# Kernel optimization log

Hardware: AMD Instinct MI355X
Metric: run time of the kernel (lower is better)

Reference implementation:

```python
import jax, jax.numpy as jnp
import numpy as np

B, S, E = 2, 2048, 1024
H = 16
D = E // H          # head dim = 64
K_TOP = 64          # top-k tokens kept per query in sparse branch
M = 256             # performer kernel feature dim
EPS = 1e-6


def setup_inputs() -> dict:
    key = jax.random.key(0)
    ks = jax.random.split(key, 16)
    sc = 0.02
    p = {
        'x': jax.random.normal(ks[0], (B, S, E), jnp.float32),
        # sparse-attention branch params
        'Wq_s': jax.random.normal(ks[1], (E, E), jnp.float32) * sc,
        'Wk_s': jax.random.normal(ks[2], (E, E), jnp.float32) * sc,
        'Wv_s': jax.random.normal(ks[3], (E, E), jnp.float32) * sc,
        'Wo_s': jax.random.normal(ks[4], (E, E), jnp.float32) * sc,
        'bq_s': jnp.zeros((E,), jnp.float32),
        'bk_s': jnp.zeros((E,), jnp.float32),
        'bv_s': jnp.zeros((E,), jnp.float32),
        'bo_s': jnp.zeros((E,), jnp.float32),
        # performer branch params
        'Wq_p': jax.random.normal(ks[5], (E, E), jnp.float32) * sc,
        'Wk_p': jax.random.normal(ks[6], (E, E), jnp.float32) * sc,
        'Wv_p': jax.random.normal(ks[7], (E, E), jnp.float32) * sc,
        'Wo_p': jax.random.normal(ks[8], (E, E), jnp.float32) * sc,
        'bo_p': jnp.zeros((E,), jnp.float32),
        'Wfeat': jax.random.normal(ks[9], (D, M), jnp.float32) / np.sqrt(D),
        # gate
        'Wg': jax.random.normal(ks[10], (E, 2), jnp.float32) * sc,
        'bg': jnp.zeros((2,), jnp.float32),
    }
    return p


def _split_heads(t):
    # [B,S,E] -> [B,H,S,D]
    return t.reshape(B, S, H, D).transpose(0, 2, 1, 3)


def _merge_heads(t):
    # [B,H,S,D] -> [B,S,E]
    return t.transpose(0, 2, 1, 3).reshape(B, S, E)


def _sparse_attn(x, Wq, bq, Wk, bk, Wv, bv, Wo, bo):
    q = _split_heads(x @ Wq + bq)
    k = _split_heads(x @ Wk + bk)
    v = _split_heads(x @ Wv + bv)
    scores = jnp.einsum('bhqd,bhkd->bhqk', q, k) / np.sqrt(D)  # [B,H,S,S]
    # keep only top-K scores per query row
    topv = jax.lax.top_k(scores, K_TOP)[0]
    thresh = topv[..., -1:]
    neg = jnp.finfo(scores.dtype).min
    masked = jnp.where(scores >= thresh, scores, neg)
    attn = jax.nn.softmax(masked, axis=-1)
    out = jnp.einsum('bhqk,bhkd->bhqd', attn, v)
    return _merge_heads(out) @ Wo + bo


def _performer_attn(x, Wq, Wk, Wv, Wo, bo, Wfeat):
    q = _split_heads(x @ Wq)
    k = _split_heads(x @ Wk)
    v = _split_heads(x @ Wv)
    # learned relu feature map (FAVOR-style linear attention)
    phi_q = jax.nn.relu(jnp.einsum('bhsd,dm->bhsm', q, Wfeat)) + EPS
    phi_k = jax.nn.relu(jnp.einsum('bhsd,dm->bhsm', k, Wfeat)) + EPS
    kv = jnp.einsum('bhsm,bhsd->bhmd', phi_k, v)      # [B,H,M,D]
    z = phi_k.sum(axis=2)                              # [B,H,M]
    num = jnp.einsum('bhsm,bhmd->bhsd', phi_q, kv)
    den = jnp.einsum('bhsm,bhm->bhs', phi_q, z)[..., None] + EPS
    return _merge_heads(num / den) @ Wo + bo


def reference(x, Wq_s, Wk_s, Wv_s, Wo_s, bq_s, bk_s, bv_s, bo_s,
              Wq_p, Wk_p, Wv_p, Wo_p, bo_p, Wfeat, Wg, bg):
    sparse_out = _sparse_attn(x, Wq_s, bq_s, Wk_s, bk_s, Wv_s, bv_s, Wo_s, bo_s)
    perf_out = _performer_attn(x, Wq_p, Wk_p, Wv_p, Wo_p, bo_p, Wfeat)
    avg_hidden = x.mean(axis=1)                        # [B,E]
    gate = jax.nn.softmax(avg_hidden @ Wg + bg, axis=-1)  # [B,2]
    w_s = gate[:, 0][:, None, None]
    w_p = gate[:, 1][:, None, None]
    # dropout is identity in eval/reference mode
    return w_s * sparse_out + w_p * perf_out
```

## Files before the change

### kernel.cpp

```cpp
#include <hip/hip_runtime.h>


constexpr int cB = 2, cS = 2048, cE = 1024, cH = 16, cD = 64, cKTOP = 64, cM = 256;
constexpr float cEPS = 1e-6f;

typedef _Float16 half8 __attribute__((ext_vector_type(8)));
typedef float f32x16 __attribute__((ext_vector_type(16)));

__device__ __forceinline__ unsigned int f2key(float f) {
    unsigned int u = __float_as_uint(f);
    return (u & 0x80000000u) ? ~u : (u | 0x80000000u);
}

__device__ __forceinline__ unsigned short h2u(_Float16 h) {
    union { _Float16 h; unsigned short u; } x; x.h = h; return x.u;
}

__device__ __forceinline__ half8 ld_half8(const unsigned short* p) {
    union { uint4 u; half8 h; } x;
    x.u = *(const uint4*)p;
    return x.h;
}

__global__ __launch_bounds__(256)
void gemm_qk2_blas(const float* __restrict__ A,
                   const float* __restrict__ Wq,
                   const float* __restrict__ Wk,
                   const float* __restrict__ bq,
                   const float* __restrict__ bk_,
                   float* __restrict__ Cq,
                   float* __restrict__ Ck,
                   unsigned short* __restrict__ khi,
                   int K, int N)
{
    __shared__ __align__(16) float As[16][68];
    __shared__ __align__(16) float Bq[16][68];
    __shared__ __align__(16) float Bk[16][68];
    const int t  = threadIdx.x;
    const int r0 = blockIdx.y * 64;
    const int c0 = blockIdx.x * 64;
    const int tm = t >> 4, tn = t & 15;
    float paccQ[4][4] = {};
    float caccQ[4][4] = {};
    float paccK[4][4] = {};
    float caccK[4][4] = {};

    const int ar = t >> 2, ak = (t & 3) * 4;
    const int bk = t >> 4, bc = (t & 15) * 4;

    for (int k0 = 0; k0 < K; k0 += 16) {
        const float4 av  = *(const float4*)(A  + (size_t)(r0 + ar) * K + (k0 + ak));
        const float4 bqv = *(const float4*)(Wq + (size_t)(k0 + bk) * N + (c0 + bc));
        const float4 bkv = *(const float4*)(Wk + (size_t)(k0 + bk) * N + (c0 + bc));
        As[ak + 0][ar] = av.x;
        As[ak + 1][ar] = av.y;
        As[ak + 2][ar] = av.z;
        As[ak + 3][ar] = av.w;
        *(float4*)&Bq[bk][bc] = bqv;
        *(float4*)&Bk[bk][bc] = bkv;
        __syncthreads();
        #pragma unroll
        for (int kk = 0; kk < 16; ++kk) {
            const float4 a4  = *(const float4*)&As[kk][tm * 4];
            const float4 q4  = *(const float4*)&Bq[kk][tn * 4];
            const float4 k4  = *(const float4*)&Bk[kk][tn * 4];
            const float a[4]  = {a4.x, a4.y, a4.z, a4.w};
            const float bqr[4] = {q4.x, q4.y, q4.z, q4.w};
            const float bkr[4] = {k4.x, k4.y, k4.z, k4.w};
            #pragma unroll
            for (int i = 0; i < 4; ++i)
                #pragma unroll
                for (int j = 0; j < 4; ++j) {
                    paccQ[i][j] = fmaf(a[i], bqr[j], paccQ[i][j]);
                    paccK[i][j] = fmaf(a[i], bkr[j], paccK[i][j]);
                }
        }
        __syncthreads();
        const int kn = k0 + 16;
        if (kn == 384 || kn == 768 || kn == K) {
            #pragma unroll
            for (int i = 0; i < 4; ++i)
                #pragma unroll
                for (int j = 0; j < 4; ++j) {
                    caccQ[i][j] = caccQ[i][j] + paccQ[i][j];
                    paccQ[i][j] = 0.f;
                    caccK[i][j] = caccK[i][j] + paccK[i][j];
                    paccK[i][j] = 0.f;
                }
        }
    }
    #pragma unroll
    for (int i = 0; i < 4; ++i) {
        const int r = r0 + tm * 4 + i;
        const int c = c0 + tn * 4;
        float4 vq;
        vq.x = caccQ[i][0] + bq[c + 0];
        vq.y = caccQ[i][1] + bq[c + 1];
        vq.z = caccQ[i][2] + bq[c + 2];
        vq.w = caccQ[i][3] + bq[c + 3];
        *(float4*)&Cq[(size_t)r * N + c] = vq;
        float4 vk;
        vk.x = caccK[i][0] + bk_[c + 0];
        vk.y = caccK[i][1] + bk_[c + 1];
        vk.z = caccK[i][2] + bk_[c + 2];
        vk.w = caccK[i][3] + bk_[c + 3];
        *(float4*)&Ck[(size_t)r * N + c] = vk;
        ushort4 hs;
        hs.x = h2u((_Float16)vk.x);
        hs.y = h2u((_Float16)vk.y);
        hs.z = h2u((_Float16)vk.z);
        hs.w = h2u((_Float16)vk.w);
        *(ushort4*)&khi[(size_t)r * N + c] = hs;
    }
}

__global__ __launch_bounds__(256)
void conv_wT(const float* __restrict__ W,
             unsigned short* __restrict__ wthi,
             unsigned short* __restrict__ wtlo)
{
    __shared__ float tile[64][68];
    const int t  = threadIdx.x;
    const int k0 = blockIdx.y * 64;
    const int n0 = blockIdx.x * 64;
    const int r  = t >> 4, c4 = (t & 15) * 4;
    #pragma unroll
    for (int i = 0; i < 4; ++i) {
        const int k = r + 16 * i;
        const float4 v = *(const float4*)&W[(size_t)(k0 + k) * cE + n0 + c4];
        tile[k][c4 + 0] = v.x; tile[k][c4 + 1] = v.y;
        tile[k][c4 + 2] = v.z; tile[k][c4 + 3] = v.w;
    }
    __syncthreads();
    #pragma unroll
    for (int i = 0; i < 4; ++i) {
        const int n = r + 16 * i;
        unsigned int hp[2], lp[2];
        #pragma unroll
        for (int p = 0; p < 2; ++p) {
            unsigned short hh[2], ll[2];
            #pragma unroll
            for (int j = 0; j < 2; ++j) {
                const float f = tile[c4 + p * 2 + j][n];
                const _Float16 h = (_Float16)f;
                hh[j] = h2u(h);
                ll[j] = h2u((_Float16)(f - (float)h));
            }
            hp[p] = (unsigned int)hh[0] | ((unsigned int)hh[1] << 16);
            lp[p] = (unsigned int)ll[0] | ((unsigned int)ll[1] << 16);
        }
        uint2 hv, lv;
        hv.x = hp[0]; hv.y = hp[1];
        lv.x = lp[0]; lv.y = lp[1];
        *(uint2*)&wthi[(size_t)(n0 + n) * cE + k0 + c4] = hv;
        *(uint2*)&wtlo[(size_t)(n0 + n) * cE + k0 + c4] = lv;
    }
}

__global__ __launch_bounds__(256)
void gemm_hilo(const float* __restrict__ A,
               const unsigned short* __restrict__ wthi,
               const unsigned short* __restrict__ wtlo,
               const float* __restrict__ bias,
               float* __restrict__ C)
{
    __shared__ __align__(16) unsigned short Ah[128][24];
    __shared__ __align__(16) unsigned short Al[128][24];
    __shared__ __align__(16) unsigned short Bh[64][24];
    __shared__ __align__(16) unsigned short Bl[64][24];

    const int t    = threadIdx.x;
    const int lane = t & 63, wave = t >> 6;
    const int wr   = wave >> 1, wc = wave & 1;
    const int r0   = blockIdx.y * 128, c0 = blockIdx.x * 64;
    const int fr   = lane & 31, g5 = lane >> 5;

    const int arow = t >> 1, aka = (t & 1) * 8;
    const int bsel = t >> 7;
    const int brow = (t & 127) >> 1, bkb = (t & 1) * 8;
    const unsigned short* wsrc = bsel ? wtlo : wthi;

    f32x16 acc0 = {0.f,0.f,0.f,0.f,0.f,0.f,0.f,0.f,0.f,0.f,0.f,0.f,0.f,0.f,0.f,0.f};
    f32x16 acc1 = {0.f,0.f,0.f,0.f,0.f,0.f,0.f,0.f,0.f,0.f,0.f,0.f,0.f,0.f,0.f,0.f};

    for (int k0 = 0; k0 < cE; k0 += 16) {
        const float4 x0 = *(const float4*)&A[(size_t)(r0 + arow) * cE + k0 + aka];
        const float4 x1 = *(const float4*)&A[(size_t)(r0 + arow) * cE + k0 + aka + 4];
        const float xf[8] = {x0.x, x0.y, x0.z, x0.w, x1.x, x1.y, x1.z, x1.w};
        unsigned int hw[4], lw[4];
        #pragma unroll
        for (int p = 0; p < 4; ++p) {
            unsigned short hh[2], ll[2];
            #pragma unroll
            for (int j = 0; j < 2; ++j) {
                const float f = xf[p * 2 + j];
                const _Float16 h = (_Float16)f;
                hh[j] = h2u(h);
                ll[j] = h2u((_Float16)(f - (float)h));
            }
            hw[p] = (unsigned int)hh[0] | ((unsigned int)hh[1] << 16);
            lw[p] = (unsigned int)ll[0] | ((unsigned int)ll[1] << 16);
        }
        uint4 hv, lv;
        hv.x = hw[0]; hv.y = hw[1]; hv.z = hw[2]; hv.w = hw[3];
        lv.x = lw[0]; lv.y = lw[1]; lv.z = lw[2]; lv.w = lw[3];
        *(uint4*)&Ah[arow][aka] = hv;
        *(uint4*)&Al[arow][aka] = lv;

        const uint4 wv = *(const uint4*)&wsrc[(size_t)(c0 + brow) * cE + k0 + bkb];
        if (bsel) *(uint4*)&Bl[brow][bkb] = wv;
        else      *(uint4*)&Bh[brow][bkb] = wv;
        __syncthreads();

        const half8 a0h = ld_half8(&Ah[wr * 64 + fr][g5 * 8]);
        const half8 a0l = ld_half8(&Al[wr * 64 + fr][g5 * 8]);
        const half8 a1h = ld_half8(&Ah[wr * 64 + 32 + fr][g5 * 8]);
        const half8 a1l = ld_half8(&Al[wr * 64 + 32 + fr][g5 * 8]);
        const half8 bh  = ld_half8(&Bh[wc * 32 + fr][g5 * 8]);
        const half8 bl  = ld_half8(&Bl[wc * 32 + fr][g5 * 8]);

        acc0 = __builtin_amdgcn_mfma_f32_32x32x16_f16(a0l, bh, acc0, 0, 0, 0);
        acc0 = __builtin_amdgcn_mfma_f32_32x32x16_f16(a0h, bl, acc0, 0, 0, 0);
        acc0 = __builtin_amdgcn_mfma_f32_32x32x16_f16(a0h, bh, acc0, 0, 0, 0);
        acc1 = __builtin_amdgcn_mfma_f32_32x32x16_f16(a1l, bh, acc1, 0, 0, 0);
        acc1 = __builtin_amdgcn_mfma_f32_32x32x16_f16(a1h, bl, acc1, 0, 0, 0);
        acc1 = __builtin_amdgcn_mfma_f32_32x32x16_f16(a1h, bh, acc1, 0, 0, 0);
        __syncthreads();
    }

    const int col = c0 + wc * 32 + fr;
    const float bv = bias ? bias[col] : 0.f;
    #pragma unroll
    for (int rg = 0; rg < 16; ++rg) {
        const int row = r0 + wr * 64 + (rg & 3) + 8 * (rg >> 2) + 4 * g5;
        C[(size_t)row * cE + col] = acc0[rg] + bv;
    }
    #pragma unroll
    for (int rg = 0; rg < 16; ++rg) {
        const int row = r0 + wr * 64 + 32 + (rg & 3) + 8 * (rg >> 2) + 4 * g5;
        C[(size_t)row * cE + col] = acc1[rg] + bv;
    }
}

__global__ __launch_bounds__(256)
void out_gemm_hilo(const float* __restrict__ As_, const float* __restrict__ Ap_,
                   const unsigned short* __restrict__ w1hi,
                   const unsigned short* __restrict__ w1lo,
                   const unsigned short* __restrict__ w2hi,
                   const unsigned short* __restrict__ w2lo,
                   const float* __restrict__ bos, const float* __restrict__ bop,
                   const float* __restrict__ gates, float* __restrict__ out)
{
    __shared__ __align__(16) unsigned short A1h[128][24], A1l[128][24];
    __shared__ __align__(16) unsigned short A2h[128][24], A2l[128][24];
    __shared__ __align__(16) unsigned short B1h[64][24],  B1l[64][24];
    __shared__ __align__(16) unsigned short B2h[64][24],  B2l[64][24];

    const int t    = threadIdx.x;
    const int lane = t & 63, wave = t >> 6;
    const int wr   = wave >> 1, wc = wave & 1;
    const int r0   = blockIdx.y * 128, c0 = blockIdx.x * 64;
    const int fr   = lane & 31, g5 = lane >> 5;
    const int b    = r0 >> 11;
    const float gs = gates[b * 2 + 0], gp = gates[b * 2 + 1];

    const int arow = t >> 1, aka = (t & 1) * 8;
    const int bsel = t >> 7;
    const int brow = (t & 127) >> 1, bkb = (t & 1) * 8;
    const unsigned short* s1 = bsel ? w1lo : w1hi;
    const unsigned short* s2 = bsel ? w2lo : w2hi;

    f32x16 acc0 = {0.f,0.f,0.f,0.f,0.f,0.f,0.f,0.f,0.f,0.f,0.f,0.f,0.f,0.f,0.f,0.f};
    f32x16 acc1 = {0.f,0.f,0.f,0.f,0.f,0.f,0.f,0.f,0.f,0.f,0.f,0.f,0.f,0.f,0.f,0.f};

    for (int k0 = 0; k0 < cE; k0 += 16) {
        {
            const float4 x0 = *(const float4*)&As_[(size_t)(r0 + arow) * cE + k0 + aka];
            const float4 x1 = *(const float4*)&As_[(size_t)(r0 + arow) * cE + k0 + aka + 4];
            const float xf[8] = {x0.x * gs, x0.y * gs, x0.z * gs, x0.w * gs,
                                 x1.x * gs, x1.y * gs, x1.z * gs, x1.w * gs};
            unsigned int hw[4], lw[4];
            #pragma unroll
            for (int p = 0; p < 4; ++p) {
                unsigned short hh[2], ll[2];
                #pragma unroll
                for (int j = 0; j < 2; ++j) {
                    const float f = xf[p * 2 + j];
                    const _Float16 h = (_Float16)f;
                    hh[j] = h2u(h);
                    ll[j] = h2u((_Float16)(f - (float)h));
                }
                hw[p] = (unsigned int)hh[0] | ((unsigned int)hh[1] << 16);
                lw[p] = (unsigned int)ll[0] | ((unsigned int)ll[1] << 16);
            }
            uint4 hv, lv;
            hv.x = hw[0]; hv.y = hw[1]; hv.z = hw[2]; hv.w = hw[3];
            lv.x = lw[0]; lv.y = lw[1]; lv.z = lw[2]; lv.w = lw[3];
            *(uint4*)&A1h[arow][aka] = hv;
            *(uint4*)&A1l[arow][aka] = lv;
        }
        {
            const float4 x0 = *(const float4*)&Ap_[(size_t)(r0 + arow) * cE + k0 + aka];
            const float4 x1 = *(const float4*)&Ap_[(size_t)(r0 + arow) * cE + k0 + aka + 4];
            const float xf[8] = {x0.x * gp, x0.y * gp, x0.z * gp, x0.w * gp,
                                 x1.x * gp, x1.y * gp, x1.z * gp, x1.w * gp};
            unsigned int hw[4], lw[4];
            #pragma unroll
            for (int p = 0; p < 4; ++p) {
                unsigned short hh[2], ll[2];
                #pragma unroll
                for (int j = 0; j < 2; ++j) {
                    const float f = xf[p * 2 + j];
                    const _Float16 h = (_Float16)f;
                    hh[j] = h2u(h);
                    ll[j] = h2u((_Float16)(f - (float)h));
                }
                hw[p] = (unsigned int)hh[0] | ((unsigned int)hh[1] << 16);
                lw[p] = (unsigned int)ll[0] | ((unsigned int)ll[1] << 16);
            }
            uint4 hv, lv;
            hv.x = hw[0]; hv.y = hw[1]; hv.z = hw[2]; hv.w = hw[3];
            lv.x = lw[0]; lv.y = lw[1]; lv.z = lw[2]; lv.w = lw[3];
            *(uint4*)&A2h[arow][aka] = hv;
            *(uint4*)&A2l[arow][aka] = lv;
        }
        {
            const uint4 w1 = *(const uint4*)&s1[(size_t)(c0 + brow) * cE + k0 + bkb];
            if (bsel) *(uint4*)&B1l[brow][bkb] = w1;
            else      *(uint4*)&B1h[brow][bkb] = w1;
            const uint4 w2 = *(const uint4*)&s2[(size_t)(c0 + brow) * cE + k0 + bkb];
            if (bsel) *(uint4*)&B2l[brow][bkb] = w2;
            else      *(uint4*)&B2h[brow][bkb] = w2;
        }
        __syncthreads();

        const half8 b1h = ld_half8(&B1h[wc * 32 + fr][g5 * 8]);
        const half8 b1l = ld_half8(&B1l[wc * 32 + fr][g5 * 8]);
        const half8 b2h = ld_half8(&B2h[wc * 32 + fr][g5 * 8]);
        const half8 b2l = ld_half8(&B2l[wc * 32 + fr][g5 * 8]);
        {
            const half8 a1h = ld_half8(&A1h[wr * 64 + fr][g5 * 8]);
            const half8 a1l = ld_half8(&A1l[wr * 64 + fr][g5 * 8]);
            const half8 a2h = ld_half8(&A2h[wr * 64 + fr][g5 * 8]);
            const half8 a2l = ld_half8(&A2l[wr * 64 + fr][g5 * 8]);
            acc0 = __builtin_amdgcn_mfma_f32_32x32x16_f16(a1l, b1h, acc0, 0, 0, 0);
            acc0 = __builtin_amdgcn_mfma_f32_32x32x16_f16(a1h, b1l, acc0, 0, 0, 0);
            acc0 = __builtin_amdgcn_mfma_f32_32x32x16_f16(a1h, b1h, acc0, 0, 0, 0);
            acc0 = __builtin_amdgcn_mfma_f32_32x32x16_f16(a2l, b2h, acc0, 0, 0, 0);
            acc0 = __builtin_amdgcn_mfma_f32_32x32x16_f16(a2h, b2l, acc0, 0, 0, 0);
            acc0 = __builtin_amdgcn_mfma_f32_32x32x16_f16(a2h, b2h, acc0, 0, 0, 0);
        }
        {
            const half8 a1h = ld_half8(&A1h[wr * 64 + 32 + fr][g5 * 8]);
            const half8 a1l = ld_half8(&A1l[wr * 64 + 32 + fr][g5 * 8]);
            const half8 a2h = ld_half8(&A2h[wr * 64 + 32 + fr][g5 * 8]);
            const half8 a2l = ld_half8(&A2l[wr * 64 + 32 + fr][g5 * 8]);
            acc1 = __builtin_amdgcn_mfma_f32_32x32x16_f16(a1l, b1h, acc1, 0, 0, 0);
            acc1 = __builtin_amdgcn_mfma_f32_32x32x16_f16(a1h, b1l, acc1, 0, 0, 0);
            acc1 = __builtin_amdgcn_mfma_f32_32x32x16_f16(a1h, b1h, acc1, 0, 0, 0);
            acc1 = __builtin_amdgcn_mfma_f32_32x32x16_f16(a2l, b2h, acc1, 0, 0, 0);
            acc1 = __builtin_amdgcn_mfma_f32_32x32x16_f16(a2h, b2l, acc1, 0, 0, 0);
            acc1 = __builtin_amdgcn_mfma_f32_32x32x16_f16(a2h, b2h, acc1, 0, 0, 0);
        }
        __syncthreads();
    }

    const int col = c0 + wc * 32 + fr;
    const float bv = gs * bos[col] + gp * bop[col];
    #pragma unroll
    for (int rg = 0; rg < 16; ++rg) {
        const int row = r0 + wr * 64 + (rg & 3) + 8 * (rg >> 2) + 4 * g5;
        out[(size_t)row * cE + col] = acc0[rg] + bv;
    }
    #pragma unroll
    for (int rg = 0; rg < 16; ++rg) {
        const int row = r0 + wr * 64 + 32 + (rg & 3) + 8 * (rg >> 2) + 4 * g5;
        out[(size_t)row * cE + col] = acc1[rg] + bv;
    }
}

__global__ __launch_bounds__(256, 4)
void sparse_attn(const float* __restrict__ Q,
                 const unsigned short* __restrict__ Khi,
                 const float* __restrict__ Ks, const float* __restrict__ V,
                 float* __restrict__ O)
{
    __shared__ float QfT[64][8];
    __shared__ __align__(16) unsigned short Qhi[8][72];
    __shared__ unsigned int hist[8][257];
    __shared__ unsigned short cidx[8][128];
    __shared__ double cval[8][128];
    __shared__ float cw[8][128];
    __shared__ int cnt[8];
    __shared__ int t16hi[8], rem[8], t16[8];
    __shared__ double T64s[8], s65s[8], rowm[8];

    const int t   = threadIdx.x;
    const int bh  = blockIdx.y;
    const int b   = bh >> 4;
    const int h64 = (bh & 15) * 64;
    const int q0  = blockIdx.x * 8;

    if (t < 128) {
        const int r = t >> 4, c4 = (t & 15) * 4;
        const float4 v =
            *(const float4*)&Q[((size_t)(b * cS + q0 + r)) * cE + h64 + c4];
        const float f[4] = {v.x, v.y, v.z, v.w};
        #pragma unroll
        for (int i = 0; i < 4; ++i) {
            QfT[c4 + i][r] = f[i];
            Qhi[r][c4 + i] = h2u((_Float16)f[i]);
        }
    }
    for (int i = t; i < 8 * 257; i += 256) (&hist[0][0])[i] = 0u;
    if (t < 8) cnt[t] = 0;
    __syncthreads();

    const int lane = t & 63;
    const int wv   = t >> 6;
    const int col  = lane & 31;
    const int g5   = lane >> 5;
    const int r0   = g5 * 4;

    half8 ahi[4];
    {
        const int arow = col & 7;
        #pragma unroll
        for (int ks = 0; ks < 4; ++ks)
            ahi[ks] = ld_half8(&Qhi[arow][g5 * 8 + ks * 16]);
    }
    unsigned int su[16][2];
    {
        const size_t kbase = ((size_t)(b * cS + wv * 512 + col)) * cE + h64;
        #pragma unroll
        for (int tl = 0; tl < 16; ++tl) {
            const unsigned short* kh = Khi + kbase + (size_t)tl * 32 * cE;
            f32x16 acc = {0.f,0.f,0.f,0.f,0.f,0.f,0.f,0.f,
                          0.f,0.f,0.f,0.f,0.f,0.f,0.f,0.f};
            #pragma unroll
            for (int ks = 0; ks < 4; ++ks) {
                const half8 bh8 = ld_half8(kh + g5 * 8 + ks * 16);
                acc = __builtin_amdgcn_mfma_f32_32x32x16_f16(ahi[ks], bh8, acc, 0, 0, 0);
            }
            const unsigned int k0 = f2key(acc[0] * 0.125f) >> 16;
            const unsigned int k1 = f2key(acc[1] * 0.125f) >> 16;
            const unsigned int k2 = f2key(acc[2] * 0.125f) >> 16;
            const unsigned int k3 = f2key(acc[3] * 0.125f) >> 16;
            su[tl][0] = k0 | (k1 << 16);
            su[tl][1] = k2 | (k3 << 16);
            atomicAdd(&hist[r0 + 0][k0 >> 8], 1u);
            atomicAdd(&hist[r0 + 1][k1 >> 8], 1u);
            atomicAdd(&hist[r0 + 2][k2 >> 8], 1u);
            atomicAdd(&hist[r0 + 3][k3 >> 8], 1u);
        }
    }
    __syncthreads();
    if (t < 8) {
        int need = cKTOP + 1;
        int hb = 0;
        for (int bin = 255; bin >= 0; --bin) {
            const int c = (int)hist[t][bin];
            if (c >= need) { hb = bin; break; }
            need -= c;
        }
        t16hi[t] = hb;
        rem[t] = need;
    }
    __syncthreads();
    for (int i = t; i < 8 * 257; i += 256) (&hist[0][0])[i] = 0u;
    __syncthreads();
    #pragma unroll
    for (int tl = 0; tl < 16; ++tl)
        #pragma unroll
        for (int w = 0; w < 2; ++w) {
            const unsigned int u = su[tl][w];
            const int rlo = r0 + 2 * w, rhi = rlo + 1;
            const unsigned int vlo = u & 0xFFFFu;
            const unsigned int vhi = u >> 16;
            if ((int)(vlo >> 8) == t16hi[rlo]) atomicAdd(&hist[rlo][vlo & 255u], 1u);
            if ((int)(vhi >> 8) == t16hi[rhi]) atomicAdd(&hist[rhi][vhi & 255u], 1u);
        }
    __syncthreads();
    if (t < 8) {
        int need = rem[t];
        int lb = 0;
        for (int bin = 255; bin >= 0; --bin) {
            const int c = (int)hist[t][bin];
            if (c >= need) { lb = bin; break; }
            need -= c;
        }
        t16[t] = (t16hi[t] << 8) | lb;
    }
    __syncthreads();

    #pragma unroll
    for (int tl = 0; tl < 16; ++tl) {
        const int key = wv * 512 + tl * 32 + col;
        #pragma unroll
        for (int w = 0; w < 2; ++w) {
            const unsigned int u = su[tl][w];
            const int rlo = r0 + 2 * w, rhi = rlo + 1;
            const int v0 = (int)(u & 0xFFFFu);
            const int v1 = (int)(u >> 16);
            if (v0 >= max(t16[rlo] - 3, 0)) {
                const int slot = atomicAdd(&cnt[rlo], 1);
                if (slot < 128) cidx[rlo][slot] = (unsigned short)key;
            }
            if (v1 >= max(t16[rhi] - 3, 0)) {
                const int slot = atomicAdd(&cnt[rhi], 1);
                if (slot < 128) cidx[rhi][slot] = (unsigned short)key;
            }
        }
    }
    __syncthreads();

    #pragma unroll
    for (int rx = 0; rx < 2; ++rx) {
        const int rr = wv * 2 + rx;
        const int n = min(cnt[rr], 128);
        for (int c = lane; c < n; c += 64) {
            const int key = cidx[rr][c];
            const float* kp = Ks + ((size_t)(b * cS + key)) * cE + h64;
            double a = 0.0;
            #pragma unroll 4
            for (int d4 = 0; d4 < 64; d4 += 4) {
                const float4 kv = *(const float4*)&kp[d4];
                a = fma((double)QfT[d4 + 0][rr], (double)kv.x, a);
                a = fma((double)QfT[d4 + 1][rr], (double)kv.y, a);
                a = fma((double)QfT[d4 + 2][rr], (double)kv.z, a);
                a = fma((double)QfT[d4 + 3][rr], (double)kv.w, a);
            }
            cval[rr][c] = a * 0.125;
        }
    }
    __syncthreads();

    #pragma unroll
    for (int rx = 0; rx < 2; ++rx) {
        const int rr = wv * 2 + rx;
        const int n = min(cnt[rr], 128);
        for (int c = lane; c < n; c += 64) {
            const double v = cval[rr][c];
            int rank = 0;
            for (int i = 0; i < n; ++i) rank += (cval[rr][i] > v) ? 1 : 0;
            if (rank == 0)  rowm[rr] = v;
            if (rank == 63) T64s[rr] = v;
            if (rank == 64) s65s[rr] = v;
        }
    }
    __syncthreads();

    #pragma unroll
    for (int rx = 0; rx < 2; ++rx) {
        const int rr = wv * 2 + rx;
        const int n = min(cnt[rr], 128);
        const double T64 = T64s[rr], s65 = s65s[rr], m = rowm[rr];
        float za = 0.f;
        for (int c = lane; c < n; c += 64) {
            const double v = cval[rr][c];
            if (v >= T64) za += expf((float)(v - m));
        }
        #pragma unroll
        for (int off = 32; off >= 1; off >>= 1)
            za += __shfl_xor(za, off);
        const float g   = (float)(T64 - s65);
        const float gm  = fmaxf(g - 5e-7f, 0.f);
        const float wB  = 0.5f * erfcf(gm * (1.0f / 2.2e-6f));
        const float wA  = 1.f - wB;
        const float e64 = expf((float)(T64 - m));
        const float e65 = expf((float)(s65 - m));
        const float ZB  = za - e64 + e65;
        const float cIn = wA / za + wB / ZB;
        const float c64 = wA / za;
        const float c65 = wB / ZB;
        for (int c = lane; c < n; c += 64) {
            const double v = cval[rr][c];
            float cc = 0.f;
            if (v > T64)       cc = cIn;
            else if (v == T64) cc = c64;
            else if (v == s65) cc = c65;
            cw[rr][c] = (cc != 0.f) ? cc * expf((float)(v - m)) : 0.f;
        }
    }
    __syncthreads();

    #pragma unroll
    for (int rx = 0; rx < 2; ++rx) {
        const int rr = wv * 2 + rx;
        const int n = min(cnt[rr], 128);
        float o = 0.f;
        int j = 0;
        for (; j + 8 <= n; j += 8) {
            float wreg[8];
            int   kreg[8];
            #pragma unroll
            for (int u = 0; u < 8; ++u) {
                wreg[u] = cw[rr][j + u];
                kreg[u] = cidx[rr][j + u];
            }
            float vreg[8];
            #pragma unroll
            for (int u = 0; u < 8; ++u)
                vreg[u] = V[((size_t)(b * cS + kreg[u])) * cE + h64 + lane];
            #pragma unroll
            for (int u = 0; u < 8; ++u)
                o = fmaf(wreg[u], vreg[u], o);
        }
        for (; j < n; ++j)
            o = fmaf(cw[rr][j],
                     V[((size_t)(b * cS + cidx[rr][j])) * cE + h64 + lane], o);
        O[((size_t)(b * cS + q0 + rr)) * cE + h64 + lane] = o;
    }
}

__global__ __launch_bounds__(256)
void perf_kv(const float* __restrict__ Kp, const float* __restrict__ Vp,
             const float* __restrict__ Wfeat,
             float* __restrict__ kvpart, float* __restrict__ zpart)
{
    __shared__ __align__(16) float Wf[64][68];
    __shared__ __align__(16) float Kt[64][68];
    __shared__ __align__(16) float Vt[64][68];
    __shared__ __align__(16) float Ph[64][68];
    const int t    = threadIdx.x;
    const int mc   = blockIdx.x & 3;
    const int sc   = blockIdx.x >> 2;
    const int bh   = blockIdx.y;
    const int b    = bh >> 4;
    const int h64  = (bh & 15) * 64;
    const int m0   = mc * 64;
    const int sbase = sc * 1024;

    #pragma unroll
    for (int i = 0; i < 4; ++i) {
        const int lin = t + 256 * i;
        const int d   = lin >> 4;
        const int m4  = (lin & 15) * 4;
        *(float4*)&Wf[d][m4] = *(const float4*)&Wfeat[d * cM + m0 + m4];
    }

    const int tm = t >> 4, tn = t & 15;
    const int sr = tm * 4;
    const int cn = tn * 4;
    float akv[4][4] = {};
    float az = 0.f;

    for (int st = 0; st < 16; ++st) {
        const int s0g = sbase + st * 64;
        __syncthreads();
        #pragma unroll
        for (int i = 0; i < 4; ++i) {
            const int row = tm + 16 * i;
            const size_t base = ((size_t)(b * cS + s0g + row)) * cE + h64 + cn;
            *(float4*)&Kt[row][cn] = *(const float4*)&Kp[base];
            *(float4*)&Vt[row][cn] = *(const float4*)&Vp[base];
        }
        __syncthreads();
        float4 p0 = {0,0,0,0}, p1 = {0,0,0,0}, p2 = {0,0,0,0}, p3 = {0,0,0,0};
        #pragma unroll 8
        for (int d = 0; d < 64; ++d) {
            const float4 wv = *(const float4*)&Wf[d][cn];
            const float k0 = Kt[sr + 0][d], k1 = Kt[sr + 1][d];
            const float k2 = Kt[sr + 2][d], k3 = Kt[sr + 3][d];
            p0.x = fmaf(k0, wv.x, p0.x); p0.y = fmaf(k0, wv.y, p0.y);
            p0.z = fmaf(k0, wv.z, p0.z); p0.w = fmaf(k0, wv.w, p0.w);
            p1.x = fmaf(k1, wv.x, p1.x); p1.y = fmaf(k1, wv.y, p1.y);
            p1.z = fmaf(k1, wv.z, p1.z); p1.w = fmaf(k1, wv.w, p1.w);
            p2.x = fmaf(k2, wv.x, p2.x); p2.y = fmaf(k2, wv.y, p2.y);
            p2.z = fmaf(k2, wv.z, p2.z); p2.w = fmaf(k2, wv.w, p2.w);
            p3.x = fmaf(k3, wv.x, p3.x); p3.y = fmaf(k3, wv.y, p3.y);
            p3.z = fmaf(k3, wv.z, p3.z); p3.w = fmaf(k3, wv.w, p3.w);
        }
        p0.x = fmaxf(p0.x, 0.f) + cEPS; p0.y = fmaxf(p0.y, 0.f) + cEPS;
        p0.z = fmaxf(p0.z, 0.f) + cEPS; p0.w = fmaxf(p0.w, 0.f) + cEPS;
        p1.x = fmaxf(p1.x, 0.f) + cEPS; p1.y = fmaxf(p1.y, 0.f) + cEPS;
        p1.z = fmaxf(p1.z, 0.f) + cEPS; p1.w = fmaxf(p1.w, 0.f) + cEPS;
        p2.x = fmaxf(p2.x, 0.f) + cEPS; p2.y = fmaxf(p2.y, 0.f) + cEPS;
        p2.z = fmaxf(p2.z, 0.f) + cEPS; p2.w = fmaxf(p2.w, 0.f) + cEPS;
        p3.x = fmaxf(p3.x, 0.f) + cEPS; p3.y = fmaxf(p3.y, 0.f) + cEPS;
        p3.z = fmaxf(p3.z, 0.f) + cEPS; p3.w = fmaxf(p3.w, 0.f) + cEPS;
        *(float4*)&Ph[sr + 0][cn] = p0;
        *(float4*)&Ph[sr + 1][cn] = p1;
        *(float4*)&Ph[sr + 2][cn] = p2;
        *(float4*)&Ph[sr + 3][cn] = p3;
        __syncthreads();
        #pragma unroll 8
        for (int ss = 0; ss < 64; ++ss) {
            const float4 pv = *(const float4*)&Ph[ss][sr];
            const float4 vv = *(const float4*)&Vt[ss][cn];
            akv[0][0] = fmaf(pv.x, vv.x, akv[0][0]); akv[0][1] = fmaf(pv.x, vv.y, akv[0][1]);
            akv[0][2] = fmaf(pv.x, vv.z, akv[0][2]); akv[0][3] = fmaf(pv.x, vv.w, akv[0][3]);
            akv[1][0] = fmaf(pv.y, vv.x, akv[1][0]); akv[1][1] = fmaf(pv.y, vv.y, akv[1][1]);
            akv[1][2] = fmaf(pv.y, vv.z, akv[1][2]); akv[1][3] = fmaf(pv.y, vv.w, akv[1][3]);
            akv[2][0] = fmaf(pv.z, vv.x, akv[2][0]); akv[2][1] = fmaf(pv.z, vv.y, akv[2][1]);
            akv[2][2] = fmaf(pv.z, vv.z, akv[2][2]); akv[2][3] = fmaf(pv.z, vv.w, akv[2][3]);
            akv[3][0] = fmaf(pv.w, vv.x, akv[3][0]); akv[3][1] = fmaf(pv.w, vv.y, akv[3][1]);
            akv[3][2] = fmaf(pv.w, vv.z, akv[3][2]); akv[3][3] = fmaf(pv.w, vv.w, akv[3][3]);
        }
        if (t < 64) {
            float a = 0.f;
            #pragma unroll 8
            for (int ss = 0; ss < 64; ++ss) a += Ph[ss][t];
            az += a;
        }
    }
    const size_t obase = ((size_t)(sc * 32 + bh)) * cM + m0;
    #pragma unroll
    for (int i = 0; i < 4; ++i) {
        float4 v; v.x = akv[i][0]; v.y = akv[i][1]; v.z = akv[i][2]; v.w = akv[i][3];
        *(float4*)&kvpart[(obase + sr + i) * cD + cn] = v;
    }
    if (t < 64) zpart[obase + t] = az;
}

__global__ __launch_bounds__(256)
void perf_numden(const float* __restrict__ Qp, const float* __restrict__ Wfeat,
                 const float* __restrict__ kvpart, const float* __restrict__ zpart,
                 float* __restrict__ Ap)
{
    __shared__ __align__(16) float Wf[64][68];
    __shared__ __align__(16) float Qt[64][68];
    __shared__ __align__(16) float KV[64][68];
    __shared__ __align__(16) float Ph[64][68];
    __shared__ __align__(16) float zl[64];
    __shared__ float den[64];
    const int t   = threadIdx.x;
    const int stb = blockIdx.x;
    const int bh  = blockIdx.y;
    const int b   = bh >> 4;
    const int h64 = (bh & 15) * 64;
    const int s0  = stb * 64;
    const int tm  = t >> 4, tn = t & 15;
    const int sr  = tm * 4, cn = tn * 4;

    #pragma unroll
    for (int i = 0; i < 4; ++i) {
        const int row = tm + 16 * i;
        *(float4*)&Qt[row][cn] =
            *(const float4*)&Qp[((size_t)(b * cS + s0 + row)) * cE + h64 + cn];
    }

    float num[4][4] = {};
    float dacc = 0.f;

    for (int mc = 0; mc < 4; ++mc) {
        const int m0 = mc * 64;
        __syncthreads();
        #pragma unroll
        for (int i = 0; i < 4; ++i) {
            const int lin = t + 256 * i;
            const int d   = lin >> 4;
            const int m4  = (lin & 15) * 4;
            *(float4*)&Wf[d][m4] = *(const float4*)&Wfeat[d * cM + m0 + m4];
        }
        #pragma unroll
        for (int i = 0; i < 4; ++i) {
            const int row = tm + 16 * i;
            const size_t o0 = ((size_t)bh * cM + m0 + row) * cD + cn;
            const size_t o1 = ((size_t)(32 + bh) * cM + m0 + row) * cD + cn;
            const float4 a = *(const float4*)&kvpart[o0];
            const float4 c = *(const float4*)&kvpart[o1];
            float4 v; v.x = a.x + c.x; v.y = a.y + c.y; v.z = a.z + c.z; v.w = a.w + c.w;
            *(float4*)&KV[row][cn] = v;
        }
        if (t < 64)
            zl[t] = zpart[(size_t)bh * cM + m0 + t] + zpart[(size_t)(32 + bh) * cM + m0 + t];
        __syncthreads();
        float4 p0 = {0,0,0,0}, p1 = {0,0,0,0}, p2 = {0,0,0,0}, p3 = {0,0,0,0};
        #pragma unroll 8
        for (int d = 0; d < 64; ++d) {
            const float4 wv = *(const float4*)&Wf[d][cn];
            const float q0 = Qt[sr + 0][d], q1 = Qt[sr + 1][d];
            const float q2 = Qt[sr + 2][d], q3 = Qt[sr + 3][d];
            p0.x = fmaf(q0, wv.x, p0.x); p0.y = fmaf(q0, wv.y, p0.y);
            p0.z = fmaf(q0, wv.z, p0.z); p0.w = fmaf(q0, wv.w, p0.w);
            p1.x = fmaf(q1, wv.x, p1.x); p1.y = fmaf(q1, wv.y, p1.y);
            p1.z = fmaf(q1, wv.z, p1.z); p1.w = fmaf(q1, wv.w, p1.w);
            p2.x = fmaf(q2, wv.x, p2.x); p2.y = fmaf(q2, wv.y, p2.y);
            p2.z = fmaf(q2, wv.z, p2.z); p2.w = fmaf(q2, wv.w, p2.w);
            p3.x = fmaf(q3, wv.x, p3.x); p3.y = fmaf(q3, wv.y, p3.y);
            p3.z = fmaf(q3, wv.z, p3.z); p3.w = fmaf(q3, wv.w, p3.w);
        }
        p0.x = fmaxf(p0.x, 0.f) + cEPS; p0.y = fmaxf(p0.y, 0.f) + cEPS;
        p0.z = fmaxf(p0.z, 0.f) + cEPS; p0.w = fmaxf(p0.w, 0.f) + cEPS;
        p1.x = fmaxf(p1.x, 0.f) + cEPS; p1.y = fmaxf(p1.y, 0.f) + cEPS;
        p1.z = fmaxf(p1.z, 0.f) + cEPS; p1.w = fmaxf(p1.w, 0.f) + cEPS;
        p2.x = fmaxf(p2.x, 0.f) + cEPS; p2.y = fmaxf(p2.y, 0.f) + cEPS;
        p2.z = fmaxf(p2.z, 0.f) + cEPS; p2.w = fmaxf(p2.w, 0.f) + cEPS;
        p3.x = fmaxf(p3.x, 0.f) + cEPS; p3.y = fmaxf(p3.y, 0.f) + cEPS;
        p3.z = fmaxf(p3.z, 0.f) + cEPS; p3.w = fmaxf(p3.w, 0.f) + cEPS;
        *(float4*)&Ph[sr + 0][cn] = p0;
        *(float4*)&Ph[sr + 1][cn] = p1;
        *(float4*)&Ph[sr + 2][cn] = p2;
        *(float4*)&Ph[sr + 3][cn] = p3;
        __syncthreads();
        #pragma unroll 8
        for (int mm = 0; mm < 64; ++mm) {
            const float4 kvv = *(const float4*)&KV[mm][cn];
            const float a0 = Ph[sr + 0][mm], a1 = Ph[sr + 1][mm];
            const float a2 = Ph[sr + 2][mm], a3 = Ph[sr + 3][mm];
            num[0][0] = fmaf(a0, kvv.x, num[0][0]); num[0][1] = fmaf(a0, kvv.y, num[0][1]);
            num[0][2] = fmaf(a0, kvv.z, num[0][2]); num[0][3] = fmaf(a0, kvv.w, num[0][3]);
            num[1][0] = fmaf(a1, kvv.x, num[1][0]); num[1][1] = fmaf(a1, kvv.y, num[1][1]);
            num[1][2] = fmaf(a1, kvv.z, num[1][2]); num[1][3] = fmaf(a1, kvv.w, num[1][3]);
            num[2][0] = fmaf(a2, kvv.x, num[2][0]); num[2][1] = fmaf(a2, kvv.y, num[2][1]);
            num[2][2] = fmaf(a2, kvv.z, num[2][2]); num[2][3] = fmaf(a2, kvv.w, num[2][3]);
            num[3][0] = fmaf(a3, kvv.x, num[3][0]); num[3][1] = fmaf(a3, kvv.y, num[3][1]);
            num[3][2] = fmaf(a3, kvv.z, num[3][2]); num[3][3] = fmaf(a3, kvv.w, num[3][3]);
        }
        if (t < 64) {
            float a = 0.f;
            #pragma unroll
            for (int m4 = 0; m4 < 64; m4 += 4) {
                const float4 ph = *(const float4*)&Ph[t][m4];
                const float4 zz = *(const float4*)&zl[m4];
                a = fmaf(ph.x, zz.x, a); a = fmaf(ph.y, zz.y, a);
                a = fmaf(ph.z, zz.z, a); a = fmaf(ph.w, zz.w, a);
            }
            dacc += a;
        }
    }
    __syncthreads();
    if (t < 64) den[t] = dacc + cEPS;
    __syncthreads();
    #pragma unroll
    for (int i = 0; i < 4; ++i) {
        const float di = 1.f / den[sr + i];
        float4 v;
        v.x = num[i][0] * di; v.y = num[i][1] * di;
        v.z = num[i][2] * di; v.w = num[i][3] * di;
        *(float4*)&Ap[((size_t)(b * cS + s0 + sr + i)) * cE + h64 + cn] = v;
    }
}

__global__ __launch_bounds__(256)
void gate_avg(const float* __restrict__ x, double* __restrict__ avgpart)
{
    const int i  = blockIdx.x * 256 + threadIdx.x;
    const int sc = blockIdx.y;
    const int b  = i >> 10, e = i & 1023;
    double acc = 0.0;
    const int sEnd = sc * 128 + 128;
    for (int s = sc * 128; s < sEnd; ++s)
        acc += (double)x[((size_t)(b * cS + s)) * cE + e];
    avgpart[(size_t)sc * 2048 + i] = acc;
}

__global__ void gate_final(const double* __restrict__ avgpart, const float* __restrict__ Wg,
                           const float* __restrict__ bg, float* __restrict__ gates)
{
    const int t = threadIdx.x;
    const int b = t >> 6, lane = t & 63;
    float l0 = 0.f, l1 = 0.f;
    for (int e = lane; e < cE; e += 64) {
        double s = 0.0;
        #pragma unroll
        for (int sc = 0; sc < 16; ++sc)
            s += avgpart[(size_t)sc * 2048 + b * 1024 + e];
        const float a = (float)(s / (double)cS);
        l0 = fmaf(a, Wg[e * 2 + 0], l0);
        l1 = fmaf(a, Wg[e * 2 + 1], l1);
    }
    for (int off = 32; off >= 1; off >>= 1) {
        l0 += __shfl_down(l0, off);
        l1 += __shfl_down(l1, off);
    }
    if (lane == 0) {
        l0 += bg[0]; l1 += bg[1];
        const float m = fmaxf(l0, l1);
        const float e0 = expf(l0 - m), e1 = expf(l1 - m);
        const float s = e0 + e1;
        gates[b * 2 + 0] = e0 / s;
        gates[b * 2 + 1] = e1 / s;
    }
}

extern "C" void kernel_launch(void* const* d_in, const int* in_sizes, int n_in,
                              void* d_out, int out_size, void* d_ws, size_t ws_size,
                              hipStream_t stream)
{
    (void)in_sizes; (void)n_in; (void)out_size; (void)ws_size;
    const float* x     = (const float*)d_in[0];
    const float* Wq_s  = (const float*)d_in[1];
    const float* Wk_s  = (const float*)d_in[2];
    const float* Wv_s  = (const float*)d_in[3];
    const float* Wo_s  = (const float*)d_in[4];
    const float* bq_s  = (const float*)d_in[5];
    const float* bk_s  = (const float*)d_in[6];
    const float* bv_s  = (const float*)d_in[7];
    const float* bo_s  = (const float*)d_in[8];
    const float* Wq_p  = (const float*)d_in[9];
    const float* Wk_p  = (const float*)d_in[10];
    const float* Wv_p  = (const float*)d_in[11];
    const float* Wo_p  = (const float*)d_in[12];
    const float* bo_p  = (const float*)d_in[13];
    const float* Wfeat = (const float*)d_in[14];
    const float* Wg    = (const float*)d_in[15];
    const float* bg    = (const float*)d_in[16];

    float* ws = (float*)d_ws;
    const size_t NRE = (size_t)cB * cS * cE;
    float* Qs    = ws;
    float* Ks    = Qs + NRE;
    float* KsT   = Ks + NRE;
    float* Vs    = KsT + NRE;
    float* Asout = Vs + NRE;
    float* kvpart = Asout + NRE;
    float* zpart  = kvpart + (size_t)2 * 32 * cM * cD;
    double* avgpart = (double*)(zpart + (size_t)2 * 32 * cM);
    float* gates = (float*)(avgpart + (size_t)16 * 2048);
    unsigned short* wthi  = (unsigned short*)(gates + 16);
    unsigned short* wtlo  = wthi + (size_t)cE * cE;
    unsigned short* wo1hi = wtlo + (size_t)cE * cE;
    unsigned short* wo1lo = wo1hi + (size_t)cE * cE;
    unsigned short* wo2hi = wo1lo + (size_t)cE * cE;
    unsigned short* wo2lo = wo2hi + (size_t)cE * cE;

    unsigned short* Khi = (unsigned short*)KsT;

    conv_wT<<<dim3(16, 16), 256, 0, stream>>>(Wo_s, wo1hi, wo1lo);
    conv_wT<<<dim3(16, 16), 256, 0, stream>>>(Wo_p, wo2hi, wo2lo);

    gemm_qk2_blas<<<dim3(16, 64), 256, 0, stream>>>(x, Wq_s, Wk_s, bq_s, bk_s,
                                                    Qs, Ks, Khi, cE, cE);
    conv_wT<<<dim3(16, 16), 256, 0, stream>>>(Wv_s, wthi, wtlo);
    gemm_hilo<<<dim3(16, 32), 256, 0, stream>>>(x, wthi, wtlo, bv_s, Vs);
    sparse_attn<<<dim3(256, 32), 256, 0, stream>>>(Qs, Khi, Ks, Vs, Asout);

    float* Qp    = Qs;
    float* Kp    = Ks;
    float* Vp    = Vs;
    float* Apout = KsT;
    conv_wT<<<dim3(16, 16), 256, 0, stream>>>(Wq_p, wthi, wtlo);
    gemm_hilo<<<dim3(16, 32), 256, 0, stream>>>(x, wthi, wtlo, nullptr, Qp);
    conv_wT<<<dim3(16, 16), 256, 0, stream>>>(Wk_p, wthi, wtlo);
    gemm_hilo<<<dim3(16, 32), 256, 0, stream>>>(x, wthi, wtlo, nullptr, Kp);
    conv_wT<<<dim3(16, 16), 256, 0, stream>>>(Wv_p, wthi, wtlo);
    gemm_hilo<<<dim3(16, 32), 256, 0, stream>>>(x, wthi, wtlo, nullptr, Vp);
    perf_kv<<<dim3(8, 32), 256, 0, stream>>>(Kp, Vp, Wfeat, kvpart, zpart);
    perf_numden<<<dim3(32, 32), 256, 0, stream>>>(Qp, Wfeat, kvpart, zpart, Apout);

    gate_avg<<<dim3(8, 16), 256, 0, stream>>>(x, avgpart);
    gate_final<<<dim3(1), 128, 0, stream>>>(avgpart, Wg, bg, gates);
    out_gemm_hilo<<<dim3(16, 32), 256, 0, stream>>>(Asout, Apout,
                                                    wo1hi, wo1lo, wo2hi, wo2lo,
                                                    bo_s, bo_p, gates,
                                                    (float*)d_out);
}
```

Baseline: 1.398 ms.

## Split sparse attention into candidate-selection and exact-attention kernels

The fused sparse attention kernel is split in two. The first kernel runs the fp16 MFMA scoring and histogram threshold search, then writes up to 128 candidate key indices and a count per query row to global memory. The second kernel reloads those candidates and does the fp64 rescoring, top-k softmax and V accumulation with a lighter shared-memory footprint, so it can use a higher occupancy bound. In exchange it adds a kernel launch and a global round trip for the candidate lists, and it grows the workspace.

```diff
diff --git a/kernel.cpp b/kernel.cpp
--- a/kernel.cpp
+++ b/kernel.cpp
@@ -380,26 +380,22 @@
 }
 
 __global__ __launch_bounds__(256, 4)
-void sparse_attn(const float* __restrict__ Q,
-                 const unsigned short* __restrict__ Khi,
-                 const float* __restrict__ Ks, const float* __restrict__ V,
-                 float* __restrict__ O)
-{
-    __shared__ float QfT[64][8];
+void sparse_sel(const float* __restrict__ Q,
+                const unsigned short* __restrict__ Khi,
+                unsigned short* __restrict__ gcidx,
+                int* __restrict__ gcnt)
+{
     __shared__ __align__(16) unsigned short Qhi[8][72];
     __shared__ unsigned int hist[8][257];
-    __shared__ unsigned short cidx[8][128];
-    __shared__ double cval[8][128];
-    __shared__ float cw[8][128];
     __shared__ int cnt[8];
     __shared__ int t16hi[8], rem[8], t16[8];
-    __shared__ double T64s[8], s65s[8], rowm[8];
 
     const int t   = threadIdx.x;
     const int bh  = blockIdx.y;
     const int b   = bh >> 4;
     const int h64 = (bh & 15) * 64;
     const int q0  = blockIdx.x * 8;
+    const size_t rid0 = ((size_t)bh * 256 + blockIdx.x) * 8;
 
     if (t < 128) {
         const int r = t >> 4, c4 = (t & 15) * 4;
@@ -407,10 +403,8 @@
             *(const float4*)&Q[((size_t)(b * cS + q0 + r)) * cE + h64 + c4];
         const float f[4] = {v.x, v.y, v.z, v.w};
         #pragma unroll
-        for (int i = 0; i < 4; ++i) {
-            QfT[c4 + i][r] = f[i];
+        for (int i = 0; i < 4; ++i)
             Qhi[r][c4 + i] = h2u((_Float16)f[i]);
-        }
     }
     for (int i = t; i < 8 * 257; i += 256) (&hist[0][0])[i] = 0u;
     if (t < 8) cnt[t] = 0;
@@ -504,15 +498,51 @@
             const int v1 = (int)(u >> 16);
             if (v0 >= max(t16[rlo] - 3, 0)) {
                 const int slot = atomicAdd(&cnt[rlo], 1);
-                if (slot < 128) cidx[rlo][slot] = (unsigned short)key;
+                if (slot < 128) gcidx[(rid0 + rlo) * 128 + slot] = (unsigned short)key;
             }
             if (v1 >= max(t16[rhi] - 3, 0)) {
                 const int slot = atomicAdd(&cnt[rhi], 1);
-                if (slot < 128) cidx[rhi][slot] = (unsigned short)key;
+                if (slot < 128) gcidx[(rid0 + rhi) * 128 + slot] = (unsigned short)key;
             }
         }
     }
     __syncthreads();
+    if (t < 8) gcnt[rid0 + t] = cnt[t];
+}
+
+__global__ __launch_bounds__(256, 8)
+void sparse_att(const float* __restrict__ Q,
+                const unsigned short* __restrict__ gcidx,
+                const int* __restrict__ gcnt,
+                const float* __restrict__ Ks, const float* __restrict__ V,
+                float* __restrict__ O)
+{
+    __shared__ float QfT[64][8];
+    __shared__ unsigned short cidx[8][128];
+    __shared__ double cval[8][128];
+    __shared__ float cw[8][128];
+    __shared__ int cnt[8];
+    __shared__ double T64s[8], s65s[8], rowm[8];
+
+    const int t   = threadIdx.x;
+    const int bh  = blockIdx.y;
+    const int b   = bh >> 4;
+    const int h64 = (bh & 15) * 64;
+    const int q0  = blockIdx.x * 8;
+    const size_t rid0 = ((size_t)bh * 256 + blockIdx.x) * 8;
+
+    if (t < 128) {
+        const int r = t >> 4, c4 = (t & 15) * 4;
+        const float4 v =
+            *(const float4*)&Q[((size_t)(b * cS + q0 + r)) * cE + h64 + c4];
+        QfT[c4 + 0][r] = v.x; QfT[c4 + 1][r] = v.y;
+        QfT[c4 + 2][r] = v.z; QfT[c4 + 3][r] = v.w;
+    }
+    ((ushort4*)&cidx[0][0])[t] = ((const ushort4*)&gcidx[rid0 * 128])[t];
+    if (t < 8) cnt[t] = gcnt[rid0 + t];
+    __syncthreads();
+
+    const int wv = t >> 6, lane = t & 63;
 
     #pragma unroll
     for (int rx = 0; rx < 2; ++rx) {
@@ -915,6 +945,8 @@
     unsigned short* wo1lo = wo1hi + (size_t)cE * cE;
     unsigned short* wo2hi = wo1lo + (size_t)cE * cE;
     unsigned short* wo2lo = wo2hi + (size_t)cE * cE;
+    unsigned short* gcidx = wo2lo + (size_t)cE * cE;
+    int* gcnt = (int*)(gcidx + (size_t)256 * 32 * 8 * 128);
 
     unsigned short* Khi = (unsigned short*)KsT;
 
@@ -925,7 +957,8 @@
                                                     Qs, Ks, Khi, cE, cE);
     conv_wT<<<dim3(16, 16), 256, 0, stream>>>(Wv_s, wthi, wtlo);
     gemm_hilo<<<dim3(16, 32), 256, 0, stream>>>(x, wthi, wtlo, bv_s, Vs);
-    sparse_attn<<<dim3(256, 32), 256, 0, stream>>>(Qs, Khi, Ks, Vs, Asout);
+    sparse_sel<<<dim3(256, 32), 256, 0, stream>>>(Qs, Khi, gcidx, gcnt);
+    sparse_att<<<dim3(256, 32), 256, 0, stream>>>(Qs, gcidx, gcnt, Ks, Vs, Asout);
 
     float* Qp    = Qs;
     float* Kp    = Ks;
```

After: 1.430 ms. 2.3% more time.
